# Performance work log

Hardware: AMD Instinct MI355X
Metric: run time of the kernel (lower is better)

Reference implementation:

```python
import jax, jax.numpy as jnp
import numpy as np

S, B, IN, H, L = 512, 64, 1024, 1024, 2


def setup_inputs() -> dict:
    key = jax.random.key(0)
    ks = jax.random.split(key, 4)
    scale = 1.0 / np.sqrt(H)
    return {
        "x": jax.random.normal(ks[0], (S, B, IN), dtype=jnp.float32),
        "h_0": jax.random.normal(ks[1], (L, B, H), dtype=jnp.float32),
        "W_i": jax.random.normal(ks[2], (L, 3, H, IN), dtype=jnp.float32) * scale,
        "W_h": jax.random.normal(ks[3], (L, 3, H, H), dtype=jnp.float32) * scale,
        "b_i": jnp.zeros((L, 3, H), dtype=jnp.float32),
        "b_h": jnp.zeros((L, 3, H), dtype=jnp.float32),
    }


def _gru_layer(x_seq, h0, Wi, Wh, bi, bh):
    # x_seq: [S,B,In]; gate order along axis 0 of Wi/Wh/bi/bh: (r, z, n)
    # Precompute all input-side projections in one big GEMM: [S,B,3H]
    gi = jnp.einsum("sbi,ghi->sbgh", x_seq, Wi) + bi  # g=3 gates
    Wh_flat = Wh.reshape(3 * Wh.shape[1], Wh.shape[2])  # [3H, H]
    bh_flat = bh.reshape(-1)

    def step(h, gi_t):
        gh = (h @ Wh_flat.T + bh_flat).reshape(h.shape[0], 3, -1)  # [B,3,H]
        r = jax.nn.sigmoid(gi_t[:, 0] + gh[:, 0])
        z = jax.nn.sigmoid(gi_t[:, 1] + gh[:, 1])
        n = jnp.tanh(gi_t[:, 2] + r * gh[:, 2])
        h_new = (1.0 - z) * n + z * h
        return h_new, h_new

    h_last, out = jax.lax.scan(step, h0, gi)
    return out, h_last  # out: [S,B,H]


def reference(x, h_0, W_i, W_h, b_i, b_h):
    h_n = []
    seq = x
    for l in range(L):
        seq, h_last = _gru_layer(seq, h_0[l], W_i[l], W_h[l], b_i[l], b_h[l])
        h_n.append(h_last)
    return seq, jnp.stack(h_n, axis=0)
```

## Files before the change

### kernel.cpp

```cpp
#include <hip/hip_runtime.h>
#include <hip/hip_bf16.h>

#define S_LEN 512
#define BATCH 64
#define H_DIM 1024
#define NLAYER 2
#define G3 3072
#define CS 128
#define CROWS (CS*BATCH)

typedef __bf16 bf16_t;
typedef __bf16 bf16x8_t __attribute__((ext_vector_type(8)));
typedef __bf16 bf16x4_t __attribute__((ext_vector_type(4)));
typedef float f32x4 __attribute__((ext_vector_type(4)));

__device__ __forceinline__ float sigmoidf_(float x) { return 1.0f / (1.0f + __expf(-x)); }

__device__ __forceinline__ void split2(float f, bf16_t& hi, bf16_t& lo) {
    hi = (bf16_t)f;
    lo = (bf16_t)(f - (float)hi);
}

__global__ void split_kernel(const float* __restrict__ in, bf16_t* __restrict__ hi,
                             bf16_t* __restrict__ lo, int n4) {
    int i = blockIdx.x * blockDim.x + threadIdx.x;
    int stride = gridDim.x * blockDim.x;
    for (; i < n4; i += stride) {
        f32x4 v = *(const f32x4*)(in + 4 * (size_t)i);
        bf16x4_t h, l;
#pragma unroll
        for (int j = 0; j < 4; ++j) { bf16_t a, b; split2(v[j], a, b); h[j] = a; l[j] = b; }
        *(bf16x4_t*)(hi + 4 * (size_t)i) = h;
        *(bf16x4_t*)(lo + 4 * (size_t)i) = l;
    }
}

__global__ __launch_bounds__(256) void proj_kernel(
    const bf16_t* __restrict__ Ah, const bf16_t* __restrict__ Al,
    const bf16_t* __restrict__ Wh, const bf16_t* __restrict__ Wl,
    const float* __restrict__ bias,
    float* __restrict__ Cout)
{
    __shared__ bf16_t sA[2][128][72];
    __shared__ bf16_t sW[2][128][72];
    const int tid = threadIdx.x;
    const int lane = tid & 63;
    const int w = tid >> 6;
    const int wm = w >> 1, wn = w & 1;
    const int bn = blockIdx.x, bm = blockIdx.y;
    const int fr = lane & 15;
    const int fq = lane >> 4;

    f32x4 acc[4][4] = {};

    const bf16_t* A0 = Ah + (size_t)bm * 128 * 1024;
    const bf16_t* A1 = Al + (size_t)bm * 128 * 1024;
    const bf16_t* W0 = Wh + (size_t)bn * 128 * 1024;
    const bf16_t* W1 = Wl + (size_t)bn * 128 * 1024;

    for (int kt = 0; kt < 16; ++kt) {
        const int k0 = kt * 64;
#pragma unroll
        for (int it = 0; it < 4; ++it) {
            int g = tid + it * 256;
            int row = g >> 3, c8 = (g & 7) * 8;
            size_t so = (size_t)row * 1024 + k0 + c8;
            *(bf16x8_t*)&sA[0][row][c8] = *(const bf16x8_t*)(A0 + so);
            *(bf16x8_t*)&sA[1][row][c8] = *(const bf16x8_t*)(A1 + so);
            *(bf16x8_t*)&sW[0][row][c8] = *(const bf16x8_t*)(W0 + so);
            *(bf16x8_t*)&sW[1][row][c8] = *(const bf16x8_t*)(W1 + so);
        }
        __syncthreads();
#pragma unroll
        for (int kk = 0; kk < 2; ++kk) {
            const int koff = kk * 32 + fq * 8;
            bf16x8_t ah[4], al[4], wh8[4], wl8[4];
#pragma unroll
            for (int mt = 0; mt < 4; ++mt) {
                ah[mt] = *(const bf16x8_t*)&sA[0][wm * 64 + mt * 16 + fr][koff];
                al[mt] = *(const bf16x8_t*)&sA[1][wm * 64 + mt * 16 + fr][koff];
            }
#pragma unroll
            for (int nt = 0; nt < 4; ++nt) {
                wh8[nt] = *(const bf16x8_t*)&sW[0][wn * 64 + nt * 16 + fr][koff];
                wl8[nt] = *(const bf16x8_t*)&sW[1][wn * 64 + nt * 16 + fr][koff];
            }
#pragma unroll
            for (int mt = 0; mt < 4; ++mt)
#pragma unroll
                for (int nt = 0; nt < 4; ++nt) {
                    acc[mt][nt] = __builtin_amdgcn_mfma_f32_16x16x32_bf16(ah[mt], wh8[nt], acc[mt][nt], 0, 0, 0);
                    acc[mt][nt] = __builtin_amdgcn_mfma_f32_16x16x32_bf16(ah[mt], wl8[nt], acc[mt][nt], 0, 0, 0);
                    acc[mt][nt] = __builtin_amdgcn_mfma_f32_16x16x32_bf16(al[mt], wh8[nt], acc[mt][nt], 0, 0, 0);
                }
        }
        __syncthreads();
    }
#pragma unroll
    for (int nt = 0; nt < 4; ++nt) {
        int n = bn * 128 + wn * 64 + nt * 16 + fr;
        float bv = bias[n];
#pragma unroll
        for (int mt = 0; mt < 4; ++mt) {
#pragma unroll
            for (int r = 0; r < 4; ++r) {
                int m = bm * 128 + wm * 64 + mt * 16 + fq * 4 + r;
                Cout[(size_t)m * G3 + n] = acc[mt][nt][r] + bv;
            }
        }
    }
}

__global__ __launch_bounds__(256) void rec_step_kernel(
    const float* __restrict__ gi_t,
    const bf16_t* __restrict__ Whh,
    const bf16_t* __restrict__ Whl,
    const float* __restrict__ bhl,
    const float* __restrict__ h_in,
    float* __restrict__ h_out,
    float* __restrict__ out_f32,
    bf16_t* __restrict__ out_hi,
    bf16_t* __restrict__ out_lo,
    float* __restrict__ hn_out)
{
    __shared__ bf16_t sH[4][2][32][72];
    __shared__ bf16_t sW[4][2][32][72];
    __shared__ float sP[4][32][32];

    const int tid = threadIdx.x;
    const int lane = tid & 63;
    const int w = tid >> 6;
    const int b0 = blockIdx.y * 32;
    const int j0 = blockIdx.x * 8;
    const int fr = lane & 15, fq = lane >> 4;

    f32x4 acc[2][2] = {};

    for (int ck = 0; ck < 4; ++ck) {
        const int k0 = w * 256 + ck * 64;
#pragma unroll
        for (int it = 0; it < 8; ++it) {
            int g = lane + it * 64;
            int row = g >> 4, c4 = (g & 15) * 4;
            f32x4 v = *(const f32x4*)(h_in + (size_t)(b0 + row) * 1024 + k0 + c4);
            bf16x4_t hh, ll;
#pragma unroll
            for (int j = 0; j < 4; ++j) { bf16_t a, b; split2(v[j], a, b); hh[j] = a; ll[j] = b; }
            *(bf16x4_t*)&sH[w][0][row][c4] = hh;
            *(bf16x4_t*)&sH[w][1][row][c4] = ll;
        }
#pragma unroll
        for (int it = 0; it < 3; ++it) {
            int g = lane + it * 64;
            int row = g >> 3, c8 = (g & 7) * 8;
            int gate = row >> 3, jj = row & 7;
            size_t so = (size_t)(gate * 1024 + j0 + jj) * 1024 + k0 + c8;
            *(bf16x8_t*)&sW[w][0][row][c8] = *(const bf16x8_t*)(Whh + so);
            *(bf16x8_t*)&sW[w][1][row][c8] = *(const bf16x8_t*)(Whl + so);
        }
#pragma unroll
        for (int kk = 0; kk < 2; ++kk) {
            const int koff = kk * 32 + fq * 8;
            bf16x8_t ah[2], al[2], wh8[2], wl8[2];
#pragma unroll
            for (int mt = 0; mt < 2; ++mt) {
                ah[mt] = *(const bf16x8_t*)&sH[w][0][mt * 16 + fr][koff];
                al[mt] = *(const bf16x8_t*)&sH[w][1][mt * 16 + fr][koff];
            }
#pragma unroll
            for (int nt = 0; nt < 2; ++nt) {
                wh8[nt] = *(const bf16x8_t*)&sW[w][0][nt * 16 + fr][koff];
                wl8[nt] = *(const bf16x8_t*)&sW[w][1][nt * 16 + fr][koff];
            }
#pragma unroll
            for (int mt = 0; mt < 2; ++mt)
#pragma unroll
                for (int nt = 0; nt < 2; ++nt) {
                    acc[mt][nt] = __builtin_amdgcn_mfma_f32_16x16x32_bf16(ah[mt], wh8[nt], acc[mt][nt], 0, 0, 0);
                    acc[mt][nt] = __builtin_amdgcn_mfma_f32_16x16x32_bf16(ah[mt], wl8[nt], acc[mt][nt], 0, 0, 0);
                    acc[mt][nt] = __builtin_amdgcn_mfma_f32_16x16x32_bf16(al[mt], wh8[nt], acc[mt][nt], 0, 0, 0);
                }
        }
    }
#pragma unroll
    for (int mt = 0; mt < 2; ++mt)
#pragma unroll
        for (int nt = 0; nt < 2; ++nt)
#pragma unroll
            for (int r = 0; r < 4; ++r)
                sP[w][mt * 16 + fq * 4 + r][nt * 16 + fr] = acc[mt][nt][r];
    __syncthreads();

    {
        const int b = tid >> 3, jj = tid & 7;
        const int bg = b0 + b, jg = j0 + jj;
        float ghr = sP[0][b][jj] + sP[1][b][jj] + sP[2][b][jj] + sP[3][b][jj];
        float ghz = sP[0][b][8 + jj] + sP[1][b][8 + jj] + sP[2][b][8 + jj] + sP[3][b][8 + jj];
        float ghn = sP[0][b][16 + jj] + sP[1][b][16 + jj] + sP[2][b][16 + jj] + sP[3][b][16 + jj];
        ghr += bhl[jg];
        ghz += bhl[1024 + jg];
        ghn += bhl[2048 + jg];
        const float* gib = gi_t + (size_t)bg * G3;
        float r = sigmoidf_(gib[jg] + ghr);
        float z = sigmoidf_(gib[1024 + jg] + ghz);
        float n = tanhf(gib[2048 + jg] + r * ghn);
        float h = h_in[(size_t)bg * 1024 + jg];
        float hn = (1.0f - z) * n + z * h;
        h_out[(size_t)bg * 1024 + jg] = hn;
        if (out_f32) out_f32[(size_t)bg * 1024 + jg] = hn;
        if (out_hi) {
            bf16_t a, bb; split2(hn, a, bb);
            out_hi[(size_t)bg * 1024 + jg] = a;
            out_lo[(size_t)bg * 1024 + jg] = bb;
        }
        if (hn_out) hn_out[(size_t)bg * 1024 + jg] = hn;
    }
}

extern "C" void kernel_launch(void* const* d_in, const int* in_sizes, int n_in,
                              void* d_out, int out_size, void* d_ws, size_t ws_size,
                              hipStream_t stream)
{
    (void)in_sizes; (void)n_in; (void)out_size;
    const float* x   = (const float*)d_in[0];
    const float* h0  = (const float*)d_in[1];
    const float* Wi  = (const float*)d_in[2];
    const float* Whw = (const float*)d_in[3];
    const float* bi  = (const float*)d_in[4];
    const float* bh  = (const float*)d_in[5];
    float* out = (float*)d_out;

    char* ws = (char*)d_ws;
    size_t off = 0;
    float*  gi    = (float*)(ws + off);  off += (size_t)CROWS * G3 * 4;
    bf16_t* sx_hi = (bf16_t*)(ws + off); off += (size_t)S_LEN * BATCH * 1024 * 2;
    bf16_t* sx_lo = (bf16_t*)(ws + off); off += (size_t)S_LEN * BATCH * 1024 * 2;
    bf16_t* wi_hi = (bf16_t*)(ws + off); off += (size_t)NLAYER * G3 * 1024 * 2;
    bf16_t* wi_lo = (bf16_t*)(ws + off); off += (size_t)NLAYER * G3 * 1024 * 2;
    bf16_t* wh_hi = (bf16_t*)(ws + off); off += (size_t)NLAYER * G3 * 1024 * 2;
    bf16_t* wh_lo = (bf16_t*)(ws + off); off += (size_t)NLAYER * G3 * 1024 * 2;
    float*  hb0   = (float*)(ws + off);  off += (size_t)BATCH * 1024 * 4;
    float*  hb1   = (float*)(ws + off);  off += (size_t)BATCH * 1024 * 4;
    if (off > ws_size) return;

    split_kernel<<<2048, 256, 0, stream>>>(x, sx_hi, sx_lo, (int)((size_t)S_LEN * BATCH * 1024 / 4));
    split_kernel<<<2048, 256, 0, stream>>>(Wi, wi_hi, wi_lo, (int)((size_t)NLAYER * G3 * 1024 / 4));
    split_kernel<<<2048, 256, 0, stream>>>(Whw, wh_hi, wh_lo, (int)((size_t)NLAYER * G3 * 1024 / 4));

    for (int l = 0; l < NLAYER; ++l) {
        const bf16_t* WiH = wi_hi + (size_t)l * G3 * 1024;
        const bf16_t* WiL = wi_lo + (size_t)l * G3 * 1024;
        const bf16_t* WhH = wh_hi + (size_t)l * G3 * 1024;
        const bf16_t* WhL = wh_lo + (size_t)l * G3 * 1024;
        const float* bil = bi + (size_t)l * G3;
        const float* bhl = bh + (size_t)l * G3;
        const float* h0l = h0 + (size_t)l * BATCH * 1024;

        for (int c = 0; c < S_LEN / CS; ++c) {
            proj_kernel<<<dim3(24, 64), 256, 0, stream>>>(
                sx_hi + (size_t)c * CROWS * 1024, sx_lo + (size_t)c * CROWS * 1024,
                WiH, WiL, bil, gi);
            for (int tt = 0; tt < CS; ++tt) {
                const int t = c * CS + tt;
                const float* hin = (t == 0) ? h0l : ((t & 1) ? hb0 : hb1);
                float* hout = (t & 1) ? hb1 : hb0;
                float* outf = (l == 1) ? (out + (size_t)t * BATCH * 1024) : nullptr;
                bf16_t* ohi = (l == 0) ? (sx_hi + (size_t)t * BATCH * 1024) : nullptr;
                bf16_t* olo = (l == 0) ? (sx_lo + (size_t)t * BATCH * 1024) : nullptr;
                float* hn = (t == S_LEN - 1)
                                ? (out + (size_t)S_LEN * BATCH * 1024 + (size_t)l * BATCH * 1024)
                                : nullptr;
                const float* git = gi + (size_t)tt * BATCH * G3;
                rec_step_kernel<<<dim3(128, 2), 256, 0, stream>>>(
                    git, WhH, WhL, bhl, hin, hout, outf, ohi, olo, hn);
            }
        }
    }
}
```

Baseline: 10.87 ms.

## Replace per-step recurrent launches with persistent chunk kernel using grid barriers

Replaces the 128 per-timestep kernel launches per chunk with a single persistent kernel per chunk. Each block keeps its slice of the split recurrent weights resident in swizzled shared memory, and blocks are synchronized between timesteps with atomic counter/flag barriers, one per batch half. Hidden state is now exchanged as bf16 hi/lo pairs in global memory, which removes the in-kernel fp32 split. The intent is to eliminate launch overhead and repeated weight reloads, at the cost of relying on all 256 blocks being co-resident and on spin-wait latency.

```diff
diff --git a/kernel.cpp b/kernel.cpp
--- a/kernel.cpp
+++ b/kernel.cpp
@@ -8,11 +8,13 @@
 #define G3 3072
 #define CS 128
 #define CROWS (CS*BATCH)
+#define BH 65536
 
 typedef __bf16 bf16_t;
 typedef __bf16 bf16x8_t __attribute__((ext_vector_type(8)));
 typedef __bf16 bf16x4_t __attribute__((ext_vector_type(4)));
 typedef float f32x4 __attribute__((ext_vector_type(4)));
+typedef unsigned int uint32;
 
 __device__ __forceinline__ float sigmoidf_(float x) { return 1.0f / (1.0f + __expf(-x)); }
 
@@ -111,109 +113,163 @@
     }
 }
 
-__global__ __launch_bounds__(256) void rec_step_kernel(
-    const float* __restrict__ gi_t,
-    const bf16_t* __restrict__ Whh,
-    const bf16_t* __restrict__ Whl,
+__global__ __launch_bounds__(512) void rec_chunk_kernel(
+    const float* __restrict__ gi,
+    const bf16_t* __restrict__ Whh, const bf16_t* __restrict__ Whl,
     const float* __restrict__ bhl,
-    const float* __restrict__ h_in,
-    float* __restrict__ h_out,
-    float* __restrict__ out_f32,
-    bf16_t* __restrict__ out_hi,
-    bf16_t* __restrict__ out_lo,
-    float* __restrict__ hn_out)
+    const bf16_t* __restrict__ h0_hi, const bf16_t* __restrict__ h0_lo,
+    bf16_t* __restrict__ sxh, bf16_t* __restrict__ sxl,
+    bf16_t* __restrict__ hbh0, bf16_t* __restrict__ hbl0,
+    bf16_t* __restrict__ hbh1, bf16_t* __restrict__ hbl1,
+    float* __restrict__ out_seq,
+    float* __restrict__ hn_out,
+    uint32* __restrict__ bar, int t0, int layer)
 {
-    __shared__ bf16_t sH[4][2][32][72];
-    __shared__ bf16_t sW[4][2][32][72];
-    __shared__ float sP[4][32][32];
+    __shared__ bf16_t sWh[24][1024];
+    __shared__ bf16_t sWl[24][1024];
+    __shared__ float sP[8][32][32];
 
     const int tid = threadIdx.x;
     const int lane = tid & 63;
     const int w = tid >> 6;
-    const int b0 = blockIdx.y * 32;
-    const int j0 = blockIdx.x * 8;
+    const int bid = blockIdx.x;
+    const int half = bid & 1;
+    const int b0 = half * 32;
+    const int j0 = (bid >> 1) * 8;
     const int fr = lane & 15, fq = lane >> 4;
 
-    f32x4 acc[2][2] = {};
-
-    for (int ck = 0; ck < 4; ++ck) {
-        const int k0 = w * 256 + ck * 64;
-#pragma unroll
-        for (int it = 0; it < 8; ++it) {
-            int g = lane + it * 64;
-            int row = g >> 4, c4 = (g & 15) * 4;
-            f32x4 v = *(const f32x4*)(h_in + (size_t)(b0 + row) * 1024 + k0 + c4);
-            bf16x4_t hh, ll;
-#pragma unroll
-            for (int j = 0; j < 4; ++j) { bf16_t a, b; split2(v[j], a, b); hh[j] = a; ll[j] = b; }
-            *(bf16x4_t*)&sH[w][0][row][c4] = hh;
-            *(bf16x4_t*)&sH[w][1][row][c4] = ll;
-        }
-#pragma unroll
-        for (int it = 0; it < 3; ++it) {
-            int g = lane + it * 64;
-            int row = g >> 3, c8 = (g & 7) * 8;
-            int gate = row >> 3, jj = row & 7;
-            size_t so = (size_t)(gate * 1024 + j0 + jj) * 1024 + k0 + c8;
-            *(bf16x8_t*)&sW[w][0][row][c8] = *(const bf16x8_t*)(Whh + so);
-            *(bf16x8_t*)&sW[w][1][row][c8] = *(const bf16x8_t*)(Whl + so);
-        }
-#pragma unroll
-        for (int kk = 0; kk < 2; ++kk) {
-            const int koff = kk * 32 + fq * 8;
-            bf16x8_t ah[2], al[2], wh8[2], wl8[2];
+    uint32* cnt  = bar + half * 32;
+    uint32* flag = bar + half * 32 + 16;
+
+    char* w0 = (char*)&sWh[0][0];
+    char* w1 = (char*)&sWl[0][0];
+
+#pragma unroll
+    for (int it = 0; it < 6; ++it) {
+        int g = tid + it * 512;
+        int row = g >> 7;
+        int c8 = (g & 127) * 8;
+        size_t so = (size_t)((row >> 3) * 1024 + j0 + (row & 7)) * 1024 + c8;
+        uint32 off = (uint32)(row * 2048 + c8 * 2) ^ (uint32)((row & 7) << 4);
+        *(bf16x8_t*)(w0 + off) = *(const bf16x8_t*)(Whh + so);
+        *(bf16x8_t*)(w1 + off) = *(const bf16x8_t*)(Whl + so);
+    }
+    __syncthreads();
+
+    const int k0 = w * 128;
+    int wr0 = fr;
+    int wr1 = (16 + fr < 24) ? (16 + fr) : 23;
+    const uint32 wb0 = (uint32)(wr0 * 2048), wx0 = (uint32)((wr0 & 7) << 4);
+    const uint32 wb1 = (uint32)(wr1 * 2048), wx1 = (uint32)((wr1 & 7) << 4);
+
+    const int pb = tid >> 3, pj = tid & 7;
+    const int pbg = b0 + pb, pjg = j0 + pj;
+    float br = 0.f, bz = 0.f, bn_ = 0.f;
+    if (tid < 256) { br = bhl[pjg]; bz = bhl[1024 + pjg]; bn_ = bhl[2048 + pjg]; }
+
+    for (int tt = 0; tt < CS; ++tt) {
+        const int t = t0 + tt;
+
+        float gr = 0.f, gz = 0.f, gn = 0.f;
+        if (tid < 256) {
+            const float* gib = gi + ((size_t)tt * 64 + pbg) * G3;
+            gr = gib[pjg]; gz = gib[1024 + pjg]; gn = gib[2048 + pjg];
+        }
+
+        if (tt > 0) {
+            if (tid == 0) {
+                while (__hip_atomic_load(flag, __ATOMIC_ACQUIRE, __HIP_MEMORY_SCOPE_AGENT) < (uint32)tt)
+                    __builtin_amdgcn_s_sleep(1);
+                __threadfence();
+            }
+            __syncthreads();
+        }
+
+        const bf16_t *hH, *hL;
+        bf16_t *sH_, *sL_;
+        if (layer == 0) {
+            hH = (t == 0) ? h0_hi : sxh + (size_t)(t - 1) * BH;
+            hL = (t == 0) ? h0_lo : sxl + (size_t)(t - 1) * BH;
+            sH_ = sxh + (size_t)t * BH;
+            sL_ = sxl + (size_t)t * BH;
+        } else {
+            hH = (t == 0) ? h0_hi : ((t & 1) ? hbh0 : hbh1);
+            hL = (t == 0) ? h0_lo : ((t & 1) ? hbl0 : hbl1);
+            sH_ = (t & 1) ? hbh1 : hbh0;
+            sL_ = (t & 1) ? hbl1 : hbl0;
+        }
+
+        bf16x8_t ah[4][2], al[4][2];
+#pragma unroll
+        for (int kk = 0; kk < 4; ++kk) {
+            const int kg = k0 + kk * 32 + fq * 8;
 #pragma unroll
             for (int mt = 0; mt < 2; ++mt) {
-                ah[mt] = *(const bf16x8_t*)&sH[w][0][mt * 16 + fr][koff];
-                al[mt] = *(const bf16x8_t*)&sH[w][1][mt * 16 + fr][koff];
-            }
-#pragma unroll
-            for (int nt = 0; nt < 2; ++nt) {
-                wh8[nt] = *(const bf16x8_t*)&sW[w][0][nt * 16 + fr][koff];
-                wl8[nt] = *(const bf16x8_t*)&sW[w][1][nt * 16 + fr][koff];
-            }
+                size_t ro = (size_t)(b0 + mt * 16 + fr) * 1024 + kg;
+                ah[kk][mt] = *(const bf16x8_t*)(hH + ro);
+                al[kk][mt] = *(const bf16x8_t*)(hL + ro);
+            }
+        }
+
+        f32x4 acc[2][2] = {};
+#pragma unroll
+        for (int kk = 0; kk < 4; ++kk) {
+            const uint32 kb = (uint32)((k0 + kk * 32 + fq * 8) * 2);
+            bf16x8_t wh8[2], wl8[2];
+            wh8[0] = *(const bf16x8_t*)(w0 + ((wb0 + kb) ^ wx0));
+            wl8[0] = *(const bf16x8_t*)(w1 + ((wb0 + kb) ^ wx0));
+            wh8[1] = *(const bf16x8_t*)(w0 + ((wb1 + kb) ^ wx1));
+            wl8[1] = *(const bf16x8_t*)(w1 + ((wb1 + kb) ^ wx1));
 #pragma unroll
             for (int mt = 0; mt < 2; ++mt)
 #pragma unroll
                 for (int nt = 0; nt < 2; ++nt) {
-                    acc[mt][nt] = __builtin_amdgcn_mfma_f32_16x16x32_bf16(ah[mt], wh8[nt], acc[mt][nt], 0, 0, 0);
-                    acc[mt][nt] = __builtin_amdgcn_mfma_f32_16x16x32_bf16(ah[mt], wl8[nt], acc[mt][nt], 0, 0, 0);
-                    acc[mt][nt] = __builtin_amdgcn_mfma_f32_16x16x32_bf16(al[mt], wh8[nt], acc[mt][nt], 0, 0, 0);
+                    bf16x8_t wh_ = nt ? wh8[1] : wh8[0];
+                    bf16x8_t wl_ = nt ? wl8[1] : wl8[0];
+                    acc[mt][nt] = __builtin_amdgcn_mfma_f32_16x16x32_bf16(ah[kk][mt], wh_, acc[mt][nt], 0, 0, 0);
+                    acc[mt][nt] = __builtin_amdgcn_mfma_f32_16x16x32_bf16(ah[kk][mt], wl_, acc[mt][nt], 0, 0, 0);
+                    acc[mt][nt] = __builtin_amdgcn_mfma_f32_16x16x32_bf16(al[kk][mt], wh_, acc[mt][nt], 0, 0, 0);
                 }
         }
-    }
-#pragma unroll
-    for (int mt = 0; mt < 2; ++mt)
-#pragma unroll
-        for (int nt = 0; nt < 2; ++nt)
-#pragma unroll
-            for (int r = 0; r < 4; ++r)
-                sP[w][mt * 16 + fq * 4 + r][nt * 16 + fr] = acc[mt][nt][r];
-    __syncthreads();
-
-    {
-        const int b = tid >> 3, jj = tid & 7;
-        const int bg = b0 + b, jg = j0 + jj;
-        float ghr = sP[0][b][jj] + sP[1][b][jj] + sP[2][b][jj] + sP[3][b][jj];
-        float ghz = sP[0][b][8 + jj] + sP[1][b][8 + jj] + sP[2][b][8 + jj] + sP[3][b][8 + jj];
-        float ghn = sP[0][b][16 + jj] + sP[1][b][16 + jj] + sP[2][b][16 + jj] + sP[3][b][16 + jj];
-        ghr += bhl[jg];
-        ghz += bhl[1024 + jg];
-        ghn += bhl[2048 + jg];
-        const float* gib = gi_t + (size_t)bg * G3;
-        float r = sigmoidf_(gib[jg] + ghr);
-        float z = sigmoidf_(gib[1024 + jg] + ghz);
-        float n = tanhf(gib[2048 + jg] + r * ghn);
-        float h = h_in[(size_t)bg * 1024 + jg];
-        float hn = (1.0f - z) * n + z * h;
-        h_out[(size_t)bg * 1024 + jg] = hn;
-        if (out_f32) out_f32[(size_t)bg * 1024 + jg] = hn;
-        if (out_hi) {
-            bf16_t a, bb; split2(hn, a, bb);
-            out_hi[(size_t)bg * 1024 + jg] = a;
-            out_lo[(size_t)bg * 1024 + jg] = bb;
-        }
-        if (hn_out) hn_out[(size_t)bg * 1024 + jg] = hn;
+
+#pragma unroll
+        for (int mt = 0; mt < 2; ++mt)
+#pragma unroll
+            for (int nt = 0; nt < 2; ++nt)
+#pragma unroll
+                for (int r = 0; r < 4; ++r)
+                    sP[w][mt * 16 + fq * 4 + r][nt * 16 + fr] = acc[mt][nt][r];
+        __syncthreads();
+
+        if (tid < 256) {
+            float s0 = 0.f, s1 = 0.f, s2 = 0.f;
+#pragma unroll
+            for (int ww = 0; ww < 8; ++ww) {
+                s0 += sP[ww][pb][pj];
+                s1 += sP[ww][pb][8 + pj];
+                s2 += sP[ww][pb][16 + pj];
+            }
+            float r = sigmoidf_(gr + s0 + br);
+            float z = sigmoidf_(gz + s1 + bz);
+            float n = tanhf(gn + r * (s2 + bn_));
+            float hprev = (float)hH[(size_t)pbg * 1024 + pjg] + (float)hL[(size_t)pbg * 1024 + pjg];
+            float hnew = (1.0f - z) * n + z * hprev;
+            bf16_t a, b2; split2(hnew, a, b2);
+            sH_[(size_t)pbg * 1024 + pjg] = a;
+            sL_[(size_t)pbg * 1024 + pjg] = b2;
+            if (out_seq) out_seq[(size_t)t * BH + (size_t)pbg * 1024 + pjg] = hnew;
+            if (t == S_LEN - 1) hn_out[(size_t)pbg * 1024 + pjg] = hnew;
+        }
+
+        if (tt < CS - 1) {
+            __syncthreads();
+            if (tid == 0) {
+                __threadfence();
+                uint32 prev = __hip_atomic_fetch_add(cnt, 1u, __ATOMIC_ACQ_REL, __HIP_MEMORY_SCOPE_AGENT);
+                if (prev == (uint32)(tt * 128 + 127))
+                    __hip_atomic_store(flag, (uint32)(tt + 1), __ATOMIC_RELEASE, __HIP_MEMORY_SCOPE_AGENT);
+            }
+        }
     }
 }
 
@@ -239,13 +295,20 @@
     bf16_t* wi_lo = (bf16_t*)(ws + off); off += (size_t)NLAYER * G3 * 1024 * 2;
     bf16_t* wh_hi = (bf16_t*)(ws + off); off += (size_t)NLAYER * G3 * 1024 * 2;
     bf16_t* wh_lo = (bf16_t*)(ws + off); off += (size_t)NLAYER * G3 * 1024 * 2;
-    float*  hb0   = (float*)(ws + off);  off += (size_t)BATCH * 1024 * 4;
-    float*  hb1   = (float*)(ws + off);  off += (size_t)BATCH * 1024 * 4;
+    bf16_t* h0s_hi = (bf16_t*)(ws + off); off += (size_t)NLAYER * BH * 2;
+    bf16_t* h0s_lo = (bf16_t*)(ws + off); off += (size_t)NLAYER * BH * 2;
+    bf16_t* hbh0  = (bf16_t*)(ws + off); off += (size_t)BH * 2;
+    bf16_t* hbl0  = (bf16_t*)(ws + off); off += (size_t)BH * 2;
+    bf16_t* hbh1  = (bf16_t*)(ws + off); off += (size_t)BH * 2;
+    bf16_t* hbl1  = (bf16_t*)(ws + off); off += (size_t)BH * 2;
+    off = (off + 255) & ~(size_t)255;
+    uint32* bar   = (uint32*)(ws + off); off += 1024;
     if (off > ws_size) return;
 
     split_kernel<<<2048, 256, 0, stream>>>(x, sx_hi, sx_lo, (int)((size_t)S_LEN * BATCH * 1024 / 4));
     split_kernel<<<2048, 256, 0, stream>>>(Wi, wi_hi, wi_lo, (int)((size_t)NLAYER * G3 * 1024 / 4));
     split_kernel<<<2048, 256, 0, stream>>>(Whw, wh_hi, wh_lo, (int)((size_t)NLAYER * G3 * 1024 / 4));
+    split_kernel<<<128, 256, 0, stream>>>(h0, h0s_hi, h0s_lo, (int)((size_t)NLAYER * BH / 4));
 
     for (int l = 0; l < NLAYER; ++l) {
         const bf16_t* WiH = wi_hi + (size_t)l * G3 * 1024;
@@ -254,26 +317,20 @@
         const bf16_t* WhL = wh_lo + (size_t)l * G3 * 1024;
         const float* bil = bi + (size_t)l * G3;
         const float* bhl = bh + (size_t)l * G3;
-        const float* h0l = h0 + (size_t)l * BATCH * 1024;
+        const bf16_t* h0H = h0s_hi + (size_t)l * BH;
+        const bf16_t* h0L = h0s_lo + (size_t)l * BH;
+        float* hn_slot = out + (size_t)S_LEN * BH + (size_t)l * BH;
 
         for (int c = 0; c < S_LEN / CS; ++c) {
             proj_kernel<<<dim3(24, 64), 256, 0, stream>>>(
                 sx_hi + (size_t)c * CROWS * 1024, sx_lo + (size_t)c * CROWS * 1024,
                 WiH, WiL, bil, gi);
-            for (int tt = 0; tt < CS; ++tt) {
-                const int t = c * CS + tt;
-                const float* hin = (t == 0) ? h0l : ((t & 1) ? hb0 : hb1);
-                float* hout = (t & 1) ? hb1 : hb0;
-                float* outf = (l == 1) ? (out + (size_t)t * BATCH * 1024) : nullptr;
-                bf16_t* ohi = (l == 0) ? (sx_hi + (size_t)t * BATCH * 1024) : nullptr;
-                bf16_t* olo = (l == 0) ? (sx_lo + (size_t)t * BATCH * 1024) : nullptr;
-                float* hn = (t == S_LEN - 1)
-                                ? (out + (size_t)S_LEN * BATCH * 1024 + (size_t)l * BATCH * 1024)
-                                : nullptr;
-                const float* git = gi + (size_t)tt * BATCH * G3;
-                rec_step_kernel<<<dim3(128, 2), 256, 0, stream>>>(
-                    git, WhH, WhL, bhl, hin, hout, outf, ohi, olo, hn);
-            }
-        }
-    }
-}
+            hipMemsetAsync(bar, 0, 1024, stream);
+            rec_chunk_kernel<<<256, 512, 0, stream>>>(
+                gi, WhH, WhL, bhl, h0H, h0L,
+                sx_hi, sx_lo, hbh0, hbl0, hbh1, hbl1,
+                (l == 1) ? out : nullptr, hn_slot,
+                bar, c * CS, l);
+        }
+    }
+}
```

After: 34.44 ms. +216.7%, slower.
